# Kernel tuning notes

Measured on AMD Instinct MI355X. Metric: run time of the kernel, lower is better.

The kernel has to match this reference:

```python
import jax, jax.numpy as jnp
import numpy as np
from jax import lax

IMAGE_SIZE = 4096.0
IOU_THRESHOLD = 0.5
SCORE_THRESHOLD = 0.05
NUM_CLASSES = 8
TILE = 512
GRID = 8          # 8x8 tiles
N_PER_TILE = 128


def setup_inputs() -> dict:
    key = jax.random.key(0)
    k1, k2, k3, k4, k5 = jax.random.split(key, 5)
    T = GRID * GRID
    N = N_PER_TILE
    # valid boxes in tile-local coords [0, TILE]
    x1 = jax.random.uniform(k1, (T, N, 2), minval=0.0, maxval=TILE - 64.0)  # (x1, y1)
    wh = jax.random.uniform(k2, (T, N, 2), minval=5.0, maxval=64.0)
    x2 = x1 + wh                                                            # (x2, y2)
    boxes = jnp.concatenate([x1, x2], axis=-1)                              # [T,N,4]
    scores = jax.random.uniform(k3, (T, N, 1), minval=0.0, maxval=1.0)
    labels = jax.random.randint(k4, (T, N, 1), 0, NUM_CLASSES).astype(jnp.float32)
    growths = jax.random.normal(k5, (T, N, 1), dtype=jnp.float32)
    tile_results = jnp.concatenate([boxes, scores, labels, growths], axis=-1)  # [T,N,7]

    rows = np.arange(T) // GRID
    cols = np.arange(T) % GRID
    tile_positions = np.stack(
        [rows * TILE, rows * TILE + TILE, cols * TILE, cols * TILE + TILE], axis=1
    ).astype(np.int32)  # (h_start, h_end, w_start, w_end)
    return {"tile_results": tile_results, "tile_positions": jnp.asarray(tile_positions)}


def _pairwise_iou(b):
    # b: [M,4] -> [M,M]
    area = (b[:, 2] - b[:, 0]) * (b[:, 3] - b[:, 1])
    lt = jnp.maximum(b[:, None, :2], b[None, :, :2])
    rb = jnp.minimum(b[:, None, 2:], b[None, :, 2:])
    wh = jnp.clip(rb - lt, 0.0)
    inter = wh[..., 0] * wh[..., 1]
    union = area[:, None] + area[None, :] - inter
    return inter / (union + 1e-8)


def reference(tile_results, tile_positions):
    T, N, _ = tile_results.shape
    M = T * N
    boxes = tile_results[..., :4]        # [T,N,4]
    scores = tile_results[..., 4]        # [T,N]
    labels = tile_results[..., 5].astype(jnp.int32)
    growths = tile_results[..., 6]

    # per-tile offset (x += w_start, y += h_start) and clamp to image
    h_start = tile_positions[:, 0].astype(boxes.dtype)[:, None, None]
    w_start = tile_positions[:, 2].astype(boxes.dtype)[:, None, None]
    offset = jnp.concatenate([w_start, h_start, w_start, h_start], axis=-1)  # [T,1,4]
    boxes = jnp.clip(boxes + offset, 0.0, IMAGE_SIZE)

    boxes = boxes.reshape(M, 4)
    scores = scores.reshape(M)
    labels = labels.reshape(M)
    growths = growths.reshape(M)

    valid = scores > SCORE_THRESHOLD
    # sort by score desc; invalid boxes pushed to the end
    sort_key = scores - 1e9 * (1.0 - valid.astype(scores.dtype))
    order = jnp.argsort(-sort_key)
    boxes_s = boxes[order]
    scores_s = scores[order]
    labels_s = labels[order]
    growths_s = growths[order]
    valid_s = valid[order]

    # per-class NMS == global NMS on class-offset boxes (cross-class IoU = 0)
    class_shift = labels_s.astype(boxes.dtype)[:, None] * (2.0 * IMAGE_SIZE)
    iou = _pairwise_iou(boxes_s + class_shift)  # [M,M], the 268MB working set

    idx = jnp.arange(M)

    def body(i, keep):
        sup = keep[i] & (iou[i] > IOU_THRESHOLD) & (idx > i)
        return keep & ~sup

    keep = lax.fori_loop(0, M, body, valid_s)

    result = jnp.concatenate(
        [boxes_s, scores_s[:, None], labels_s.astype(boxes.dtype)[:, None], growths_s[:, None]],
        axis=1,
    )
    # fixed-shape output: suppressed / filtered rows zeroed, keep mask returned
    return result * keep[:, None].astype(result.dtype), keep
```

## Files before the change

### kernel.cpp

```cpp
#include <hip/hip_runtime.h>

#define NB       128
#define M_TOTAL  8192
#define HALF_M   4096
#define RESULT_FLOATS (M_TOTAL * 7)

typedef unsigned long long u64;
typedef unsigned int u32;

__global__ __launch_bounds__(512) void fused_nms_kernel(
    const float* __restrict__ tr,
    const int*   __restrict__ tp,
    float*       __restrict__ out)
{
    __shared__ alignas(16) u64 s_aug[HALF_M];
    __shared__ u64   s_laug[NB];
    __shared__ float t_x1[NB], t_y1[NB], t_x2[NB], t_y2[NB], t_area[NB];
    __shared__ alignas(16) u32 sup32[NB][4];
    __shared__ u64   validmask[2];
    __shared__ u64   keepmask[2];
    __shared__ int   s_cnt[512];
    __shared__ int   s_p[NB];

    const int tid = threadIdx.x;
    const int sub = blockIdx.x & 3;
    const int tb  = blockIdx.x >> 2;
    const int g0  = tb * NB;

    if (tid < 2) validmask[tid] = 0ull;

    const int n16  = tid >> 4;
    const int part = tid & 15;
    const int ibox = g0 + sub * 32 + n16;
    u64 myaug;
    {
        float sc = tr[(size_t)ibox * 7 + 4];
        u32 sb = (sc > 0.05f) ? __float_as_uint(sc) : 0u;
        myaug = ((u64)sb << 13) | (u64)(M_TOTAL - 1 - ibox);
    }

    float sx1 = 0.f, sy1 = 0.f, sx2 = 0.f, sy2 = 0.f, area = 0.f;
    u64 aug_n = 0;
    bool valid = false;
    if (tid < NB) {
        const float* row = tr + (size_t)(g0 + tid) * 7;
        float x1 = row[0], y1 = row[1], x2 = row[2], y2 = row[3];
        float score = row[4], label = row[5];
        float hf = (float)tp[tb * 4 + 0];
        float wf = (float)tp[tb * 4 + 2];
        float gx1 = fminf(fmaxf(__fadd_rn(x1, wf), 0.0f), 4096.0f);
        float gy1 = fminf(fmaxf(__fadd_rn(y1, hf), 0.0f), 4096.0f);
        float gx2 = fminf(fmaxf(__fadd_rn(x2, wf), 0.0f), 4096.0f);
        float gy2 = fminf(fmaxf(__fadd_rn(y2, hf), 0.0f), 4096.0f);
        valid = score > 0.05f;
        u32 sb = valid ? __float_as_uint(score) : 0u;
        aug_n = ((u64)sb << 13) | (u64)(M_TOTAL - 1 - (g0 + tid));
        float c = __fmul_rn(label, 8192.0f);
        sx1 = __fadd_rn(gx1, c);
        sy1 = __fadd_rn(gy1, c);
        sx2 = __fadd_rn(gx2, c);
        sy2 = __fadd_rn(gy2, c);
        area = __fmul_rn(__fsub_rn(sx2, sx1), __fsub_rn(sy2, sy1));
        s_laug[tid] = aug_n;
    }

#pragma unroll
    for (int x = 0; x < 8; ++x) {
        int j = tid + 512 * x;
        float sc = tr[(size_t)j * 7 + 4];
        u32 sb = (sc > 0.05f) ? __float_as_uint(sc) : 0u;
        s_aug[j] = ((u64)sb << 13) | (u64)(M_TOTAL - 1 - j);
    }
    __syncthreads();

    int cnt = 0;
    {
        const ulonglong2* av = (const ulonglong2*)s_aug;
#pragma unroll 4
        for (int k = 0; k < 128; ++k) {
            ulonglong2 v = av[part + 16 * k];
            cnt += (v.x > myaug) + (v.y > myaug);
        }
    }

    int p = 0;
    if (tid < NB) {
#pragma unroll 8
        for (int u = 0; u < NB; ++u) p += (s_laug[u] > aug_n);
    }
    __syncthreads();

    if (tid < NB) {
        t_x1[p] = sx1; t_y1[p] = sy1; t_x2[p] = sx2; t_y2[p] = sy2;
        t_area[p] = area;
        s_p[tid] = p;
        if (valid) atomicOr(&validmask[p >> 6], 1ull << (p & 63));
    }
#pragma unroll
    for (int x = 0; x < 8; ++x) {
        int L = tid + 512 * x;
        int j = HALF_M + L;
        float sc = tr[(size_t)j * 7 + 4];
        u32 sb = (sc > 0.05f) ? __float_as_uint(sc) : 0u;
        s_aug[L] = ((u64)sb << 13) | (u64)(M_TOTAL - 1 - j);
    }
    __syncthreads();

    {
        const ulonglong2* av = (const ulonglong2*)s_aug;
#pragma unroll 4
        for (int k = 0; k < 128; ++k) {
            ulonglong2 v = av[part + 16 * k];
            cnt += (v.x > myaug) + (v.y > myaug);
        }
    }
    s_cnt[tid] = cnt;

    {
        int r = tid >> 2, cq = tid & 3;
        float rx1 = t_x1[r], ry1 = t_y1[r], rx2 = t_x2[r], ry2 = t_y2[r];
        float ra = t_area[r];
        u32 m = 0;
        int wbase = cq * 32;
#pragma unroll 4
        for (int w2 = 0; w2 < 32; ++w2) {
            int w = wbase + w2;
            float ltx = fmaxf(rx1, t_x1[w]);
            float lty = fmaxf(ry1, t_y1[w]);
            float rbx = fminf(rx2, t_x2[w]);
            float rby = fminf(ry2, t_y2[w]);
            float iw = fmaxf(__fsub_rn(rbx, ltx), 0.0f);
            float ih = fmaxf(__fsub_rn(rby, lty), 0.0f);
            float inter = __fmul_rn(iw, ih);
            float uni   = __fsub_rn(__fadd_rn(ra, t_area[w]), inter);
            float denom = __fadd_rn(uni, 1e-8f);
            float iou   = __fdiv_rn(inter, denom);
            bool s = (w > r) && (iou > 0.5f);
            m |= ((u32)s) << w2;
        }
        sup32[r][cq] = m;
    }
    __syncthreads();

    if (tid == 0) {
        const ulonglong2* supv = (const ulonglong2*)sup32;
        u64 v0 = validmask[0], v1 = validmask[1];
        u64 r0 = 0ull, r1 = 0ull;
        for (int c = 0; c < NB; c += 8) {
            ulonglong2 buf[8];
#pragma unroll
            for (int x = 0; x < 8; ++x) buf[x] = supv[c + x];
#pragma unroll
            for (int x = 0; x < 8; ++x) {
                int q = c + x;
                u64 alive = ((q < 64) ? ((v0 & ~r0) >> q)
                                      : ((v1 & ~r1) >> (q - 64))) & 1ull;
                u64 take = 0ull - alive;
                r0 |= buf[x].x & take;
                r1 |= buf[x].y & take;
            }
        }
        keepmask[0] = v0 & ~r0;
        keepmask[1] = v1 & ~r1;
    }
    __syncthreads();

    if (tid < 32) {
        int nl = sub * 32 + tid;
        int i  = g0 + nl;
        int rank = 0;
#pragma unroll
        for (int x = 0; x < 16; ++x) rank += s_cnt[tid * 16 + x];

        int pp = s_p[nl];
        float kf = ((keepmask[pp >> 6] >> (pp & 63)) & 1ull) ? 1.0f : 0.0f;

        const float* row = tr + (size_t)i * 7;
        float x1 = row[0], y1 = row[1], x2 = row[2], y2 = row[3];
        float score = row[4], label = row[5], growth = row[6];
        float hf = (float)tp[tb * 4 + 0];
        float wf = (float)tp[tb * 4 + 2];
        float gx1 = fminf(fmaxf(__fadd_rn(x1, wf), 0.0f), 4096.0f);
        float gy1 = fminf(fmaxf(__fadd_rn(y1, hf), 0.0f), 4096.0f);
        float gx2 = fminf(fmaxf(__fadd_rn(x2, wf), 0.0f), 4096.0f);
        float gy2 = fminf(fmaxf(__fadd_rn(y2, hf), 0.0f), 4096.0f);

        float* o = out + (size_t)rank * 7;
        o[0] = __fmul_rn(gx1, kf);
        o[1] = __fmul_rn(gy1, kf);
        o[2] = __fmul_rn(gx2, kf);
        o[3] = __fmul_rn(gy2, kf);
        o[4] = __fmul_rn(score, kf);
        o[5] = __fmul_rn(label, kf);
        o[6] = __fmul_rn(growth, kf);
        out[RESULT_FLOATS + rank] = kf;
    }
}

extern "C" void kernel_launch(void* const* d_in, const int* in_sizes, int n_in,
                              void* d_out, int out_size, void* d_ws, size_t ws_size,
                              hipStream_t stream) {
    const float* tile_results   = (const float*)d_in[0];
    const int*   tile_positions = (const int*)d_in[1];
    float* out = (float*)d_out;

    hipLaunchKernelGGL(fused_nms_kernel, dim3(256), dim3(512), 0, stream,
                       tile_results, tile_positions, out);
}
```

Measured before the change: 75.48 us.

## Compute global ranks from register-held scores with wave-shuffle reductions

Instead of staging all 8192 sort keys in shared memory in two halves and having 16 threads per box scan them, each thread loads 16 scores into registers and compares them against the block's 32 target keys held in registers. Counts are packed two per 32-bit word, summed across each wave with xor shuffles, and written per wave to a small shared array. The final rank is the sum over the 8 waves. This removes the large shared-memory key array, two of the barriers and the LDS-bound scan, at the cost of many more registers (scores, 32 keys, 32 counters) and 16-bit packed counts that are bounded by 8192.

Measured after the change: 71.98 us. -4.6%, faster.

```diff
diff --git a/kernel.cpp b/kernel.cpp
--- a/kernel.cpp
+++ b/kernel.cpp
@@ -2,7 +2,6 @@
 
 #define NB       128
 #define M_TOTAL  8192
-#define HALF_M   4096
 #define RESULT_FLOATS (M_TOTAL * 7)
 
 typedef unsigned long long u64;
@@ -13,13 +12,13 @@
     const int*   __restrict__ tp,
     float*       __restrict__ out)
 {
-    __shared__ alignas(16) u64 s_aug[HALF_M];
+    __shared__ u64   s_boxaug[32];
     __shared__ u64   s_laug[NB];
     __shared__ float t_x1[NB], t_y1[NB], t_x2[NB], t_y2[NB], t_area[NB];
     __shared__ alignas(16) u32 sup32[NB][4];
     __shared__ u64   validmask[2];
     __shared__ u64   keepmask[2];
-    __shared__ int   s_cnt[512];
+    __shared__ alignas(16) u32 s_wpart[8][16];
     __shared__ int   s_p[NB];
 
     const int tid = threadIdx.x;
@@ -29,14 +28,16 @@
 
     if (tid < 2) validmask[tid] = 0ull;
 
-    const int n16  = tid >> 4;
-    const int part = tid & 15;
-    const int ibox = g0 + sub * 32 + n16;
-    u64 myaug;
-    {
-        float sc = tr[(size_t)ibox * 7 + 4];
-        u32 sb = (sc > 0.05f) ? __float_as_uint(sc) : 0u;
-        myaug = ((u64)sb << 13) | (u64)(M_TOTAL - 1 - ibox);
+    float sc[16];
+#pragma unroll
+    for (int k = 0; k < 16; ++k)
+        sc[k] = tr[(size_t)(tid + 512 * k) * 7 + 4];
+
+    if (tid < 32) {
+        int i = g0 + sub * 32 + tid;
+        float s = tr[(size_t)i * 7 + 4];
+        u32 sb = (s > 0.05f) ? __float_as_uint(s) : 0u;
+        s_boxaug[tid] = ((u64)sb << 13) | (u64)(M_TOTAL - 1 - i);
     }
 
     float sx1 = 0.f, sy1 = 0.f, sx2 = 0.f, sy2 = 0.f, area = 0.f;
@@ -63,58 +64,60 @@
         area = __fmul_rn(__fsub_rn(sx2, sx1), __fsub_rn(sy2, sy1));
         s_laug[tid] = aug_n;
     }
-
-#pragma unroll
-    for (int x = 0; x < 8; ++x) {
-        int j = tid + 512 * x;
-        float sc = tr[(size_t)j * 7 + 4];
-        u32 sb = (sc > 0.05f) ? __float_as_uint(sc) : 0u;
-        s_aug[j] = ((u64)sb << 13) | (u64)(M_TOTAL - 1 - j);
-    }
-    __syncthreads();
-
-    int cnt = 0;
-    {
-        const ulonglong2* av = (const ulonglong2*)s_aug;
-#pragma unroll 4
-        for (int k = 0; k < 128; ++k) {
-            ulonglong2 v = av[part + 16 * k];
-            cnt += (v.x > myaug) + (v.y > myaug);
-        }
-    }
-
-    int p = 0;
+    __syncthreads();
+
+    u64 bk[32];
+#pragma unroll
+    for (int b = 0; b < 32; ++b) bk[b] = s_boxaug[b];
+
     if (tid < NB) {
+        int p = 0;
+        const ulonglong2* lv = (const ulonglong2*)s_laug;
 #pragma unroll 8
-        for (int u = 0; u < NB; ++u) p += (s_laug[u] > aug_n);
-    }
-    __syncthreads();
-
-    if (tid < NB) {
+        for (int u = 0; u < 64; ++u) {
+            ulonglong2 v = lv[u];
+            p += (v.x > aug_n) + (v.y > aug_n);
+        }
         t_x1[p] = sx1; t_y1[p] = sy1; t_x2[p] = sx2; t_y2[p] = sy2;
         t_area[p] = area;
         s_p[tid] = p;
         if (valid) atomicOr(&validmask[p >> 6], 1ull << (p & 63));
     }
-#pragma unroll
-    for (int x = 0; x < 8; ++x) {
-        int L = tid + 512 * x;
-        int j = HALF_M + L;
-        float sc = tr[(size_t)j * 7 + 4];
-        u32 sb = (sc > 0.05f) ? __float_as_uint(sc) : 0u;
-        s_aug[L] = ((u64)sb << 13) | (u64)(M_TOTAL - 1 - j);
-    }
-    __syncthreads();
-
+
+    int cnt[32];
+#pragma unroll
+    for (int b = 0; b < 32; ++b) cnt[b] = 0;
+#pragma unroll
+    for (int k = 0; k < 16; ++k) {
+        int j = tid + 512 * k;
+        u32 sb = (sc[k] > 0.05f) ? __float_as_uint(sc[k]) : 0u;
+        u64 a = ((u64)sb << 13) | (u64)(M_TOTAL - 1 - j);
+#pragma unroll
+        for (int b = 0; b < 32; ++b) cnt[b] += (a > bk[b]);
+    }
+
+    u32 pk[16];
+#pragma unroll
+    for (int q = 0; q < 16; ++q)
+        pk[q] = (u32)cnt[q] | ((u32)cnt[q + 16] << 16);
+
+#pragma unroll
+    for (int q = 0; q < 16; ++q) {
+        int c = (int)pk[q];
+#pragma unroll
+        for (int m = 1; m < 64; m <<= 1) c += __shfl_xor(c, m, 64);
+        pk[q] = (u32)c;
+    }
     {
-        const ulonglong2* av = (const ulonglong2*)s_aug;
-#pragma unroll 4
-        for (int k = 0; k < 128; ++k) {
-            ulonglong2 v = av[part + 16 * k];
-            cnt += (v.x > myaug) + (v.y > myaug);
-        }
-    }
-    s_cnt[tid] = cnt;
+        const int lane = tid & 63, wv = tid >> 6;
+        if (lane == 0) {
+            uint4* wp = (uint4*)&s_wpart[wv][0];
+#pragma unroll
+            for (int q4 = 0; q4 < 4; ++q4)
+                wp[q4] = make_uint4(pk[4*q4], pk[4*q4+1], pk[4*q4+2], pk[4*q4+3]);
+        }
+    }
+    __syncthreads();
 
     {
         int r = tid >> 2, cq = tid & 3;
@@ -166,12 +169,15 @@
     __syncthreads();
 
     if (tid < 32) {
+        int rank = 0;
+        const int q = tid & 15;
+        const int sh = (tid >> 4) << 4;
+#pragma unroll
+        for (int w = 0; w < 8; ++w)
+            rank += (int)((s_wpart[w][q] >> sh) & 0xffffu);
+
         int nl = sub * 32 + tid;
         int i  = g0 + nl;
-        int rank = 0;
-#pragma unroll
-        for (int x = 0; x < 16; ++x) rank += s_cnt[tid * 16 + x];
-
         int pp = s_p[nl];
         float kf = ((keepmask[pp >> 6] >> (pp & 63)) & 1ull) ? 1.0f : 0.0f;
 
```
